# Kernel tuning notes

Hardware: AMD Instinct MI355X
Metric: run time of the kernel (lower is better)

The kernel has to match this reference:

```python
import jax, jax.numpy as jnp
import numpy as np

B, T, I, D = 64, 128, 197, 768
FP16_MAX_NEG = -jnp.finfo(jnp.float16).max  # max_neg_value(fp16) = -65504


def setup_inputs() -> dict:
    key = jax.random.key(0)
    k1, k2, k3 = jax.random.split(key, 3)
    image_features = jax.random.normal(k1, (B, I, D), dtype=jnp.float32)
    text_features = jax.random.normal(k2, (B, T, D), dtype=jnp.float32)
    # realistic padding: each text has a random valid length in [T//2, T)
    lengths = jax.random.randint(k3, (B,), T // 2, T)
    padding_mask = (jnp.arange(T)[None, :] >= lengths[:, None]).astype(jnp.int32)
    logit_scale = jnp.ones((1,), dtype=jnp.float32)
    return {
        "image_features": image_features,
        "text_features": text_features,
        "padding_mask": padding_mask,
        "logit_scale": logit_scale,
    }


def _mask_eos(pm):
    # (pm==0).cumsum(1).argmax(1) = index of LAST zero (argmax returns first max)
    cum = jnp.cumsum((pm == 0).astype(jnp.int32), axis=1)
    last_zero = jnp.argmax(cum, axis=1)
    return pm.at[jnp.arange(pm.shape[0]), last_zero].set(1)


def _cmli(image_features, text_features, padding_mask, logit_scale):
    pm = _mask_eos(padding_mask)
    img = image_features.astype(jnp.float16)[:, 1:]   # [B, I-1, D]
    txt = text_features.astype(jnp.float16)[:, 1:]    # [B, T-1, D]
    pad = pm[:, 1:].astype(bool)                       # [B, T-1], True = padded

    scale = jnp.asarray(logit_scale, dtype=jnp.float16).reshape(())
    # sim[x, y, t, i] = <text token t of sample x, image patch i of sample y>
    sim = scale * jnp.einsum('xtd,yid->xyti', txt, img)  # [B, B, T-1, I-1] fp16

    # ---- text -> image: max over image patches, masked mean over text tokens
    t2i_tok = jnp.max(sim, axis=-1)                       # [x, y, t]
    mask_xt = pad[:, None, :]                             # [x, 1, t]
    numer = jnp.sum(jnp.where(mask_xt, jnp.float16(0.0), t2i_tok), axis=-1)
    denom = jnp.maximum(
        jnp.sum(~pad, axis=-1).astype(t2i_tok.dtype), jnp.float16(1e-6)
    )[:, None]                                            # [x, 1]
    t2i = numer / denom                                   # [B, B]

    # ---- image -> text: mask padded text tokens to -max, max over t, mean over i
    masked_sim = jnp.where(pad[:, None, :, None], jnp.float16(FP16_MAX_NEG), sim)
    i2t = jnp.mean(jnp.max(masked_sim, axis=2), axis=-1)  # [B, B]
    return i2t, t2i


def _cross_entropy_diag(logits):
    # labels = arange(B): diagonal positives; compute log_softmax in fp32
    logp = jax.nn.log_softmax(logits.astype(jnp.float32), axis=-1)
    n = logits.shape[0]
    return -jnp.mean(logp[jnp.arange(n), jnp.arange(n)])


def reference(image_features, text_features, padding_mask, logit_scale):
    i2t, t2i = _cmli(image_features, text_features, padding_mask, logit_scale)
    loss = (_cross_entropy_diag(i2t) + _cross_entropy_diag(t2i)) / 2
    return loss, i2t, t2i
```

## Files before the change

### kernel.cpp

```cpp
#include <hip/hip_runtime.h>
#include <stdint.h>

#define BB   64
#define TSEQ 128
#define ISEQ 197
#define DD   768
#define TM   127
#define IM   196
#define NK   24
#define A_KB (TM*64)
#define B_KB (IM*64)

#define LDS_B0   16384
#define LDS_RK   59392
#define LDS_CK   59904
#define LDS_PT   60800
#define LDS_TOT  60864

typedef float    f32x4 __attribute__((ext_vector_type(4)));
typedef _Float16 h8    __attribute__((ext_vector_type(8)));
typedef _Float16 h4    __attribute__((ext_vector_type(4)));
typedef float    fvec4 __attribute__((ext_vector_type(4)));

__device__ __forceinline__ unsigned fkey(float f){
  unsigned u = __float_as_uint(f);
  return (u & 0x80000000u) ? ~u : (u | 0x80000000u);
}
__device__ __forceinline__ float fdekey(unsigned k){
  unsigned u = (k & 0x80000000u) ? (k & 0x7fffffffu) : ~k;
  return __uint_as_float(u);
}
__device__ __forceinline__ float waveSum(float v){
  #pragma unroll
  for (int s = 1; s < 64; s <<= 1) v += __shfl_xor(v, s, 64);
  return v;
}

__device__ __forceinline__ void gload_lds16(const void* g, void* l){
  __builtin_amdgcn_global_load_lds(
      (const __attribute__((address_space(1))) void*)g,
      (__attribute__((address_space(3))) void*)l, 16, 0, 0);
}

__global__ void mask_kernel(const int* __restrict__ pmG, float* __restrict__ bias,
                            float* __restrict__ sel, int* __restrict__ cnt)
{
  int b = blockIdx.x; int l = threadIdx.x;
  const int* row = pmG + b*TSEQ;
  int p0 = row[l]; int p1 = row[l+64];
  unsigned long long m0 = __ballot(p0 == 0);
  unsigned long long m1 = __ballot(p1 == 0);
  int lz = 0;
  if (m1)      lz = 64 + (63 - __clzll(m1));
  else if (m0) lz = 63 - __clzll(m0);
  int t1 = l + 1;
  int q1 = row[t1];
  bool v1 = (q1 == 0) && (t1 != lz);
  int t2 = l + 65;
  bool v2 = false;
  if (t2 < TSEQ){ int q2 = row[t2]; v2 = (q2 == 0) && (t2 != lz); }
  bias[b*128 + l]      = v1 ? 0.f : -3.0e38f;
  sel [b*128 + l]      = v1 ? 1.f : 0.f;
  bias[b*128 + 64 + l] = v2 ? 0.f : -3.0e38f;
  sel [b*128 + 64 + l] = v2 ? 1.f : 0.f;
  unsigned long long vm1 = __ballot(v1);
  unsigned long long vm2 = __ballot(v2);
  if (l == 0) cnt[b] = __popcll(vm1) + __popcll(vm2);
}

__global__ void cvt_txt_kernel(const float* __restrict__ src, _Float16* __restrict__ dst){
  int t = blockIdx.x;
  int b = blockIdx.y;
  int i = threadIdx.x;
  const fvec4* s = (const fvec4*)(src + ((size_t)b*TSEQ + t + 1)*DD) + i;
  fvec4 v = *s;
  h4 h; h.x=(_Float16)v.x; h.y=(_Float16)v.y; h.z=(_Float16)v.z; h.w=(_Float16)v.w;
  int ks = i >> 3; int o = (i & 7)*4;
  _Float16* d = dst + (size_t)b*(NK*TM*32) + (size_t)ks*(TM*32) + t*32 + o;
  *(h4*)d = h;
}
__global__ void cvt_img_kernel(const float* __restrict__ src, _Float16* __restrict__ dst){
  int t = blockIdx.x;
  int b = blockIdx.y;
  int i = threadIdx.x;
  const fvec4* s = (const fvec4*)(src + ((size_t)b*ISEQ + t + 1)*DD) + i;
  fvec4 v = *s;
  h4 h; h.x=(_Float16)v.x; h.y=(_Float16)v.y; h.z=(_Float16)v.z; h.w=(_Float16)v.w;
  int ks = i >> 3; int o = (i & 7)*4;
  _Float16* d = dst + (size_t)b*(NK*IM*32) + (size_t)ks*(IM*32) + t*32 + o;
  *(h4*)d = h;
}

__global__ __launch_bounds__(256, 2)
void cmli_pair_kernel(const _Float16* __restrict__ txtH,
                      const _Float16* __restrict__ imgH,
                      const float* __restrict__ biasG,
                      const float* __restrict__ selG,
                      const int* __restrict__ cntG,
                      const float* __restrict__ scaleP,
                      float* __restrict__ out)
{
  __shared__ __align__(16) char smem[LDS_TOT];
  unsigned* rowKeys = (unsigned*)(smem + LDS_RK);
  unsigned* colKeys = (unsigned*)(smem + LDS_CK);
  float*    parts   = (float*)(smem + LDS_PT);

  const int tid  = threadIdx.x;
  const int lane = tid & 63;
  const int w    = tid >> 6;
  const int wm   = w & 1;
  const int wn   = w >> 1;
  const int bx   = blockIdx.x >> 6;
  const int by   = blockIdx.x & 63;

  const char* tA = (const char*)txtH + (size_t)bx * (NK*A_KB);
  const char* tB = (const char*)imgH + (size_t)by * (NK*B_KB);
  const int mtc = (cntG[bx] + 15) >> 4;

  int aSrc[2], aLds[2];
  #pragma unroll
  for (int i=0;i<2;i++){
    int c = w + 4*i; int p = c*64 + lane; int r = p>>2; int pg = p&3;
    int g = pg ^ ((r>>1)&3);
    aSrc[i] = min(r,126)*64 + g*16; aLds[i] = c*1024;
  }
  const int kB = (w < 2) ? 4 : 3;
  int bSrc[4], bLds[4];
  #pragma unroll
  for (int i=0;i<4;i++){
    int c = w + 4*i; if (c > 13) c = 13;
    int p = c*64 + lane; int r = p>>2; int pg = p&3;
    int g = pg ^ ((r>>1)&3);
    bSrc[i] = min(r,195)*64 + g*16; bLds[i] = c*1024;
  }

  const int pgf  = (lane>>4) ^ ((lane>>1)&3);
  const int aOff = (lane&15)*64 + pgf*16;
  const int bOff = (wn*112 + (lane&15))*64 + pgf*16;

  f32x4 acc[4][7];
  #pragma unroll
  for (int j=0;j<4;j++)
    #pragma unroll
    for (int n=0;n<7;n++)
      acc[j][n] = (f32x4){0.f,0.f,0.f,0.f};

  if (tid < 128) rowKeys[tid] = 0u;
  if (tid < 224) colKeys[tid] = 0u;

  {
    #pragma unroll
    for (int i=0;i<4;i++) if (i < kB) gload_lds16(tB + bSrc[i], smem + LDS_B0 + bLds[i]);
    #pragma unroll
    for (int i=0;i<2;i++) gload_lds16(tA + aSrc[i], smem + aLds[i]);
    const char* bt1 = tB + B_KB;
    #pragma unroll
    for (int i=0;i<4;i++) if (i < kB) gload_lds16(bt1 + bSrc[i], smem + LDS_B0 + 14336 + bLds[i]);
    if (w < 2) asm volatile("s_waitcnt vmcnt(4)" ::: "memory");
    else       asm volatile("s_waitcnt vmcnt(3)" ::: "memory");
    __builtin_amdgcn_s_barrier();
    asm volatile("" ::: "memory");
  }

  int rbA = 0, rbB = 0;
  for (int t=0; t<NK; t++){
    {
      int ka  = (t+1 < NK) ? t+1 : NK-1;
      int kb2 = (t+2 < NK) ? t+2 : NK-1;
      const char* at = tA + (size_t)ka  * A_KB;
      const char* bt = tB + (size_t)kb2 * B_KB;
      int aBase = (rbA ^ 1) * 8192;
      int sb3 = rbB + 2; if (sb3 >= 3) sb3 -= 3;
      int bBase = LDS_B0 + sb3 * 14336;
      #pragma unroll
      for (int i=0;i<2;i++) gload_lds16(at + aSrc[i], smem + aBase + aLds[i]);
      #pragma unroll
      for (int i=0;i<4;i++) if (i < kB) gload_lds16(bt + bSrc[i], smem + bBase + bLds[i]);
    }
    const char* Ab = smem + rbA*8192;
    const char* Bb = smem + LDS_B0 + rbB*14336;
    h8 af[4]; h8 bf[7];
    #pragma unroll
    for (int n=0;n<7;n++) bf[n] = *(const h8*)(Bb + bOff + n*1024);
    #pragma unroll
    for (int j=0;j<4;j++){
      int g = wm + 2*j;
      if (g < mtc) af[j] = *(const h8*)(Ab + aOff + g*1024);
    }
    #pragma unroll
    for (int j=0;j<4;j++){
      int g = wm + 2*j;
      if (g < mtc){
        #pragma unroll
        for (int n=0;n<7;n++)
          acc[j][n] = __builtin_amdgcn_mfma_f32_16x16x32_f16(af[j], bf[n], acc[j][n], 0,0,0);
      }
    }
    if (w < 2) asm volatile("s_waitcnt vmcnt(4)" ::: "memory");
    else       asm volatile("s_waitcnt vmcnt(3)" ::: "memory");
    __builtin_amdgcn_s_barrier();
    asm volatile("" ::: "memory");
    rbA ^= 1; rbB = (rbB == 2) ? 0 : rbB + 1;
  }

  const float scale = scaleP[0];
  #pragma unroll
  for (int j=0;j<4;j++){
    int g = wm + 2*j;
    if (g < mtc){
      #pragma unroll
      for (int n=0;n<7;n++) acc[j][n] *= scale;
    }
  }

  #pragma unroll
  for (int j=0;j<4;j++){
    int g = wm + 2*j;
    if (g < mtc){
      f32x4 r = acc[j][0];
      #pragma unroll
      for (int n=1;n<7;n++){
        r.x = fmaxf(r.x, acc[j][n].x); r.y = fmaxf(r.y, acc[j][n].y);
        r.z = fmaxf(r.z, acc[j][n].z); r.w = fmaxf(r.w, acc[j][n].w);
      }
      #pragma unroll
      for (int s=1;s<16;s<<=1){
        r.x = fmaxf(r.x, __shfl_xor(r.x, s, 64));
        r.y = fmaxf(r.y, __shfl_xor(r.y, s, 64));
        r.z = fmaxf(r.z, __shfl_xor(r.z, s, 64));
        r.w = fmaxf(r.w, __shfl_xor(r.w, s, 64));
      }
      if ((lane & 15) == 0){
        int row = g*16 + (lane>>4)*4;
        atomicMax(&rowKeys[row+0], fkey(r.x));
        atomicMax(&rowKeys[row+1], fkey(r.y));
        atomicMax(&rowKeys[row+2], fkey(r.z));
        atomicMax(&rowKeys[row+3], fkey(r.w));
      }
    }
  }

  fvec4 bv[4];
  #pragma unroll
  for (int j=0;j<4;j++){
    int g = wm + 2*j;
    if (g < mtc)
      bv[j] = *(const fvec4*)(biasG + bx*128 + g*16 + (lane>>4)*4);
  }
  #pragma unroll
  for (int n=0;n<7;n++){
    float c = -3.0e38f;
    #pragma unroll
    for (int j=0;j<4;j++){
      int g = wm + 2*j;
      if (g < mtc){
        c = fmaxf(c, acc[j][n].x + bv[j].x);
        c = fmaxf(c, acc[j][n].y + bv[j].y);
        c = fmaxf(c, acc[j][n].z + bv[j].z);
        c = fmaxf(c, acc[j][n].w + bv[j].w);
      }
    }
    c = fmaxf(c, __shfl_xor(c, 16, 64));
    c = fmaxf(c, __shfl_xor(c, 32, 64));
    if (lane < 16){
      int col = wn*112 + n*16 + lane;
      atomicMax(&colKeys[col], fkey(c));
    }
  }
  __syncthreads();

  float v = 0.f;
  if (tid < 128){
    float s = selG[bx*128 + tid];
    v = (s > 0.5f) ? fdekey(rowKeys[tid]) : 0.f;
  }
  float u = (tid < IM) ? fdekey(colKeys[tid]) : 0.f;
  v = waveSum(v); u = waveSum(u);
  if (lane == 0){ parts[w] = v; parts[4+w] = u; }
  __syncthreads();
  if (tid == 0){
    float numer = parts[0]+parts[1]+parts[2]+parts[3];
    float csum  = parts[4]+parts[5]+parts[6]+parts[7];
    float denom = fmaxf((float)cntG[bx], 1e-6f);
    out[1 + 4096 + blockIdx.x] = numer / denom;
    out[1 + blockIdx.x]        = csum * (1.f/196.f);
  }
}

__global__ void loss_kernel(float* __restrict__ out){
  __shared__ float p[2];
  int w = threadIdx.x >> 6, lane = threadIdx.x & 63;
  const float* M = out + 1 + w*4096;
  const float* r = M + lane*64;
  float mx = -3.0e38f;
  for (int j=0;j<64;j++) mx = fmaxf(mx, r[j]);
  float se = 0.f;
  for (int j=0;j<64;j++) se += __expf(r[j]-mx);
  float nll = (mx + __logf(se)) - r[lane];
  float s = waveSum(nll);
  if (lane == 0) p[w] = s;
  __syncthreads();
  if (threadIdx.x == 0) out[0] = (p[0] + p[1]) * (0.5f/64.f);
}

extern "C" void kernel_launch(void* const* d_in, const int* in_sizes, int n_in,
                              void* d_out, int out_size, void* d_ws, size_t ws_size,
                              hipStream_t stream)
{
  const float* imgF   = (const float*)d_in[0];
  const float* txtF   = (const float*)d_in[1];
  const int*   pm     = (const int*)d_in[2];
  const float* scaleP = (const float*)d_in[3];
  float* out = (float*)d_out;

  char* ws = (char*)d_ws;
  _Float16* txtH = (_Float16*)ws;
  _Float16* imgH = (_Float16*)(ws + 12484608);
  float* bias = (float*)(ws + 31752192);
  float* sel  = (float*)(ws + 31784960);
  int*   cnt  = (int*)(ws + 31817728);

  hipLaunchKernelGGL(mask_kernel,    dim3(BB),      dim3(64),  0, stream, pm, bias, sel, cnt);
  hipLaunchKernelGGL(cvt_txt_kernel, dim3(TM, BB),  dim3(192), 0, stream, txtF, txtH);
  hipLaunchKernelGGL(cvt_img_kernel, dim3(IM, BB),  dim3(192), 0, stream, imgF, imgH);
  hipLaunchKernelGGL(cmli_pair_kernel, dim3(BB*BB), dim3(256), 0, stream,
                     txtH, imgH, bias, sel, cnt, scaleP, out);
  hipLaunchKernelGGL(loss_kernel,    dim3(1),       dim3(128), 0, stream, out);
}
```

Measured before the change: 201.2 us.

## Split K-step into two interleaved MFMA phases with setprio and unrolled buffer rotation

Restructures the GEMM main loop into a macro-expanded, six-step unrolled schedule with compile-time buffer indices. Each K step is split into two halves: the A loads and the first three B fragments feed a first MFMA batch, then the next B tile's global-to-LDS loads are issued and the remaining fragments feed a second batch. Scheduling barriers and s_setprio are added around the MFMA bursts so that loads overlap with compute and the waves stay in step. It adds extra barriers per step, which could cost synchronisation time, and duplicates a lot of code.

```diff
diff --git a/kernel.cpp b/kernel.cpp
--- a/kernel.cpp
+++ b/kernel.cpp
@@ -91,6 +91,65 @@
   *(h4*)d = h;
 }
 
+#define KSTEP(AC, BC, AN, BN2, ATP, BTP)                                      \
+  {                                                                           \
+                     \
+    gload_lds16((ATP) + aSrc[0], smem + (AN)*8192 + aLds[0]);                 \
+    gload_lds16((ATP) + aSrc[1], smem + (AN)*8192 + aLds[1]);                 \
+    const char* Ab = smem + (AC)*8192;                                        \
+    const char* Bb = smem + LDS_B0 + (BC)*14336;                              \
+    h8 af[4]; h8 bf[7];                                                       \
+    _Pragma("unroll")                                                         \
+    for (int j=0;j<4;j++){                                                    \
+      int g = wm + 2*j;                                                       \
+      if (g < mtc) af[j] = *(const h8*)(Ab + aOff + g*1024);                  \
+    }                                                                         \
+    _Pragma("unroll")                                                         \
+    for (int n=0;n<3;n++) bf[n] = *(const h8*)(Bb + bOff + n*1024);           \
+    __builtin_amdgcn_sched_barrier(0);                                        \
+    __builtin_amdgcn_s_barrier();                                             \
+    asm volatile("s_waitcnt lgkmcnt(0)" ::: "memory");                        \
+    __builtin_amdgcn_sched_barrier(0);                                        \
+    __builtin_amdgcn_s_setprio(1);                                            \
+    _Pragma("unroll")                                                         \
+    for (int j=0;j<4;j++){                                                    \
+      int g = wm + 2*j;                                                       \
+      if (g < mtc){                                                           \
+        _Pragma("unroll")                                                     \
+        for (int n=0;n<3;n++)                                                 \
+          acc[j][n] = __builtin_amdgcn_mfma_f32_16x16x32_f16(af[j], bf[n], acc[j][n], 0,0,0); \
+      }                                                                       \
+    }                                                                         \
+    __builtin_amdgcn_s_setprio(0);                                            \
+    __builtin_amdgcn_sched_barrier(0);                                        \
+    __builtin_amdgcn_s_barrier();                                             \
+                               \
+    _Pragma("unroll")                                                         \
+    for (int i=0;i<4;i++)                                                     \
+      if (i < kB) gload_lds16((BTP) + bSrc[i], smem + LDS_B0 + (BN2)*14336 + bLds[i]); \
+    _Pragma("unroll")                                                         \
+    for (int n=3;n<7;n++) bf[n] = *(const h8*)(Bb + bOff + n*1024);           \
+    __builtin_amdgcn_sched_barrier(0);                                        \
+    __builtin_amdgcn_s_barrier();                                             \
+    asm volatile("s_waitcnt lgkmcnt(0)" ::: "memory");                        \
+    __builtin_amdgcn_sched_barrier(0);                                        \
+    __builtin_amdgcn_s_setprio(1);                                            \
+    _Pragma("unroll")                                                         \
+    for (int j=0;j<4;j++){                                                    \
+      int g = wm + 2*j;                                                       \
+      if (g < mtc){                                                           \
+        _Pragma("unroll")                                                     \
+        for (int n=3;n<7;n++)                                                 \
+          acc[j][n] = __builtin_amdgcn_mfma_f32_16x16x32_f16(af[j], bf[n], acc[j][n], 0,0,0); \
+      }                                                                       \
+    }                                                                         \
+    __builtin_amdgcn_s_setprio(0);                                            \
+    __builtin_amdgcn_sched_barrier(0);                                        \
+    if (w < 2) asm volatile("s_waitcnt vmcnt(4)" ::: "memory");               \
+    else       asm volatile("s_waitcnt vmcnt(3)" ::: "memory");               \
+    __builtin_amdgcn_s_barrier();                                             \
+  }
+
 __global__ __launch_bounds__(256, 2)
 void cmli_pair_kernel(const _Float16* __restrict__ txtH,
                       const _Float16* __restrict__ imgH,
@@ -159,48 +218,28 @@
     if (w < 2) asm volatile("s_waitcnt vmcnt(4)" ::: "memory");
     else       asm volatile("s_waitcnt vmcnt(3)" ::: "memory");
     __builtin_amdgcn_s_barrier();
-    asm volatile("" ::: "memory");
-  }
-
-  int rbA = 0, rbB = 0;
-  for (int t=0; t<NK; t++){
-    {
-      int ka  = (t+1 < NK) ? t+1 : NK-1;
-      int kb2 = (t+2 < NK) ? t+2 : NK-1;
-      const char* at = tA + (size_t)ka  * A_KB;
-      const char* bt = tB + (size_t)kb2 * B_KB;
-      int aBase = (rbA ^ 1) * 8192;
-      int sb3 = rbB + 2; if (sb3 >= 3) sb3 -= 3;
-      int bBase = LDS_B0 + sb3 * 14336;
-      #pragma unroll
-      for (int i=0;i<2;i++) gload_lds16(at + aSrc[i], smem + aBase + aLds[i]);
-      #pragma unroll
-      for (int i=0;i<4;i++) if (i < kB) gload_lds16(bt + bSrc[i], smem + bBase + bLds[i]);
-    }
-    const char* Ab = smem + rbA*8192;
-    const char* Bb = smem + LDS_B0 + rbB*14336;
-    h8 af[4]; h8 bf[7];
-    #pragma unroll
-    for (int n=0;n<7;n++) bf[n] = *(const h8*)(Bb + bOff + n*1024);
-    #pragma unroll
-    for (int j=0;j<4;j++){
-      int g = wm + 2*j;
-      if (g < mtc) af[j] = *(const h8*)(Ab + aOff + g*1024);
-    }
-    #pragma unroll
-    for (int j=0;j<4;j++){
-      int g = wm + 2*j;
-      if (g < mtc){
-        #pragma unroll
-        for (int n=0;n<7;n++)
-          acc[j][n] = __builtin_amdgcn_mfma_f32_16x16x32_f16(af[j], bf[n], acc[j][n], 0,0,0);
-      }
-    }
-    if (w < 2) asm volatile("s_waitcnt vmcnt(4)" ::: "memory");
-    else       asm volatile("s_waitcnt vmcnt(3)" ::: "memory");
-    __builtin_amdgcn_s_barrier();
-    asm volatile("" ::: "memory");
-    rbA ^= 1; rbB = (rbB == 2) ? 0 : rbB + 1;
+  }
+
+  const char* aN = tA + A_KB;
+  const char* bN = tB + 2*(size_t)B_KB;
+  #pragma unroll 1
+  for (int r=0; r<3; r++){
+    KSTEP(0,0,1,2, aN, bN); aN += A_KB; bN += B_KB;
+    KSTEP(1,1,0,0, aN, bN); aN += A_KB; bN += B_KB;
+    KSTEP(0,2,1,1, aN, bN); aN += A_KB; bN += B_KB;
+    KSTEP(1,0,0,2, aN, bN); aN += A_KB; bN += B_KB;
+    KSTEP(0,1,1,0, aN, bN); aN += A_KB; bN += B_KB;
+    KSTEP(1,2,0,1, aN, bN); aN += A_KB; bN += B_KB;
+  }
+  {
+    const char* aLast = tA + (size_t)(NK-1)*A_KB;
+    const char* bLast = tB + (size_t)(NK-1)*B_KB;
+    KSTEP(0,0,1,2, aN, bN); aN += A_KB; bN += B_KB;
+    KSTEP(1,1,0,0, aN, bN); aN += A_KB; bN += B_KB;
+    KSTEP(0,2,1,1, aN, bN); aN += A_KB; bN += B_KB;
+    KSTEP(1,0,0,2, aN, bN); aN += A_KB;
+    KSTEP(0,1,1,0, aN, bLast);
+    KSTEP(1,2,0,1, aLast, bLast);
   }
 
   const float scale = scaleP[0];
```

Measured after the change: 395.5 us. 1.97x slower.

## Load text operand straight to registers and split the MFMA loop into prioritized phases

Applied to the files above, without the earlier changes.

The text (A) operand is no longer staged through LDS. Each wave reads its A fragments directly from global memory into registers, double-buffered across k-steps, and LDS is left holding only the triple-buffered image tiles. The main loop is split into two halves (B columns 0-3 and 4-6), each separated by barriers and wrapped in s_setprio, so LDS reads and MFMA issue interleave across waves. The aim is to cut LDS traffic and footprint and improve overlap, at the cost of more barriers. The prefetch pointers are no longer clamped, so the last iterations read past the end of each operand's k-range.

```diff
diff --git a/kernel.cpp b/kernel.cpp
--- a/kernel.cpp
+++ b/kernel.cpp
@@ -11,11 +11,10 @@
 #define A_KB (TM*64)
 #define B_KB (IM*64)
 
-#define LDS_B0   16384
-#define LDS_RK   59392
-#define LDS_CK   59904
-#define LDS_PT   60800
-#define LDS_TOT  60864
+#define LDS_RK   43008
+#define LDS_CK   43520
+#define LDS_PT   44416
+#define LDS_TOT  44480
 
 typedef float    f32x4 __attribute__((ext_vector_type(4)));
 typedef _Float16 h8    __attribute__((ext_vector_type(8)));
@@ -117,14 +116,6 @@
   const char* tB = (const char*)imgH + (size_t)by * (NK*B_KB);
   const int mtc = (cntG[bx] + 15) >> 4;
 
-  int aSrc[2], aLds[2];
-  #pragma unroll
-  for (int i=0;i<2;i++){
-    int c = w + 4*i; int p = c*64 + lane; int r = p>>2; int pg = p&3;
-    int g = pg ^ ((r>>1)&3);
-    aSrc[i] = min(r,126)*64 + g*16; aLds[i] = c*1024;
-  }
-  const int kB = (w < 2) ? 4 : 3;
   int bSrc[4], bLds[4];
   #pragma unroll
   for (int i=0;i<4;i++){
@@ -135,8 +126,14 @@
   }
 
   const int pgf  = (lane>>4) ^ ((lane>>1)&3);
-  const int aOff = (lane&15)*64 + pgf*16;
   const int bOff = (wn*112 + (lane&15))*64 + pgf*16;
+
+  int aG[4];
+  #pragma unroll
+  for (int j=0;j<4;j++){
+    int row = (wm + 2*j)*16 + (lane&15);
+    aG[j] = min(row,126)*64 + (lane>>4)*16;
+  }
 
   f32x4 acc[4][7];
   #pragma unroll
@@ -148,59 +145,72 @@
   if (tid < 128) rowKeys[tid] = 0u;
   if (tid < 224) colKeys[tid] = 0u;
 
+  h8 af_cur[4], af_nxt[4];
+
   {
     #pragma unroll
-    for (int i=0;i<4;i++) if (i < kB) gload_lds16(tB + bSrc[i], smem + LDS_B0 + bLds[i]);
-    #pragma unroll
-    for (int i=0;i<2;i++) gload_lds16(tA + aSrc[i], smem + aLds[i]);
-    const char* bt1 = tB + B_KB;
-    #pragma unroll
-    for (int i=0;i<4;i++) if (i < kB) gload_lds16(bt1 + bSrc[i], smem + LDS_B0 + 14336 + bLds[i]);
-    if (w < 2) asm volatile("s_waitcnt vmcnt(4)" ::: "memory");
-    else       asm volatile("s_waitcnt vmcnt(3)" ::: "memory");
-    __builtin_amdgcn_s_barrier();
-    asm volatile("" ::: "memory");
-  }
-
-  int rbA = 0, rbB = 0;
+    for (int i=0;i<4;i++) gload_lds16(tB + bSrc[i], smem + bLds[i]);
+    #pragma unroll
+    for (int j=0;j<4;j++) af_cur[j] = *(const h8*)(tA + aG[j]);
+    const char* b1 = tB + B_KB;
+    #pragma unroll
+    for (int i=0;i<4;i++) gload_lds16(b1 + bSrc[i], smem + 14336 + bLds[i]);
+    asm volatile("s_waitcnt vmcnt(4)" ::: "memory");
+    __builtin_amdgcn_s_barrier();
+  }
+
+  const char* aPtr = tA + A_KB;
+  const char* bPtr = tB + 2*(size_t)B_KB;
+  int rbB = 0;
   for (int t=0; t<NK; t++){
-    {
-      int ka  = (t+1 < NK) ? t+1 : NK-1;
-      int kb2 = (t+2 < NK) ? t+2 : NK-1;
-      const char* at = tA + (size_t)ka  * A_KB;
-      const char* bt = tB + (size_t)kb2 * B_KB;
-      int aBase = (rbA ^ 1) * 8192;
-      int sb3 = rbB + 2; if (sb3 >= 3) sb3 -= 3;
-      int bBase = LDS_B0 + sb3 * 14336;
-      #pragma unroll
-      for (int i=0;i<2;i++) gload_lds16(at + aSrc[i], smem + aBase + aLds[i]);
-      #pragma unroll
-      for (int i=0;i<4;i++) if (i < kB) gload_lds16(bt + bSrc[i], smem + bBase + bLds[i]);
-    }
-    const char* Ab = smem + rbA*8192;
-    const char* Bb = smem + LDS_B0 + rbB*14336;
-    h8 af[4]; h8 bf[7];
-    #pragma unroll
-    for (int n=0;n<7;n++) bf[n] = *(const h8*)(Bb + bOff + n*1024);
-    #pragma unroll
-    for (int j=0;j<4;j++){
-      int g = wm + 2*j;
-      if (g < mtc) af[j] = *(const h8*)(Ab + aOff + g*1024);
-    }
+    const char* Bb = smem + rbB*14336;
+    int sb = rbB + 2; if (sb >= 3) sb -= 3;
+    char* Sb = smem + sb*14336;
+
+    #pragma unroll
+    for (int j=0;j<4;j++) af_nxt[j] = *(const h8*)(aPtr + aG[j]);
+    #pragma unroll
+    for (int i=0;i<4;i++) gload_lds16(bPtr + bSrc[i], Sb + bLds[i]);
+    h8 bf[7];
+    #pragma unroll
+    for (int n=0;n<4;n++) bf[n] = *(const h8*)(Bb + bOff + n*1024);
+    __builtin_amdgcn_s_barrier();
+    __builtin_amdgcn_s_setprio(1);
     #pragma unroll
     for (int j=0;j<4;j++){
       int g = wm + 2*j;
       if (g < mtc){
         #pragma unroll
-        for (int n=0;n<7;n++)
-          acc[j][n] = __builtin_amdgcn_mfma_f32_16x16x32_f16(af[j], bf[n], acc[j][n], 0,0,0);
-      }
-    }
-    if (w < 2) asm volatile("s_waitcnt vmcnt(4)" ::: "memory");
-    else       asm volatile("s_waitcnt vmcnt(3)" ::: "memory");
-    __builtin_amdgcn_s_barrier();
-    asm volatile("" ::: "memory");
-    rbA ^= 1; rbB = (rbB == 2) ? 0 : rbB + 1;
+        for (int n=0;n<4;n++)
+          acc[j][n] = __builtin_amdgcn_mfma_f32_16x16x32_f16(af_cur[j], bf[n], acc[j][n], 0,0,0);
+      }
+    }
+    __builtin_amdgcn_s_setprio(0);
+    __builtin_amdgcn_sched_barrier(0);
+    __builtin_amdgcn_s_barrier();
+
+    #pragma unroll
+    for (int n=4;n<7;n++) bf[n] = *(const h8*)(Bb + bOff + n*1024);
+    __builtin_amdgcn_s_barrier();
+    __builtin_amdgcn_s_setprio(1);
+    #pragma unroll
+    for (int j=0;j<4;j++){
+      int g = wm + 2*j;
+      if (g < mtc){
+        #pragma unroll
+        for (int n=4;n<7;n++)
+          acc[j][n] = __builtin_amdgcn_mfma_f32_16x16x32_f16(af_cur[j], bf[n], acc[j][n], 0,0,0);
+      }
+    }
+    __builtin_amdgcn_s_setprio(0);
+    __builtin_amdgcn_sched_barrier(0);
+    asm volatile("s_waitcnt vmcnt(4)" ::: "memory");
+    __builtin_amdgcn_s_barrier();
+
+    #pragma unroll
+    for (int j=0;j<4;j++) af_cur[j] = af_nxt[j];
+    aPtr += A_KB; bPtr += B_KB;
+    rbB++; if (rbB >= 3) rbB = 0;
   }
 
   const float scale = scaleP[0];
```

After: 260.4 us. 1.29x slower.
